# Performance work log

Hardware: AMD Instinct MI355X
Metric: run time of the kernel (lower is better)

Reference implementation:

```python
import jax, jax.numpy as jnp
import numpy as np

EPS = 1e-8  # torch.cosine_similarity default eps


def setup_inputs() -> dict:
    key = jax.random.key(0)
    k1, k2, k3, k4 = jax.random.split(key, 4)
    S, M, N, D = 512, 256, 100000, 1024
    query_hidden = jax.random.normal(k1, (S, D), dtype=jnp.float32)
    bank = jax.random.normal(k2, (N, D), dtype=jnp.float32)
    bank_labels = jax.random.uniform(k3, (N,), dtype=jnp.float32)
    bucket_idx = jax.random.randint(k4, (S, M), 0, N, dtype=jnp.int64)
    return {
        "query_hidden": query_hidden,
        "bank": bank,
        "bank_labels": bank_labels,
        "bucket_idx": bucket_idx,
        "k": 5,
    }


def reference(query_hidden, bank, bank_labels, bucket_idx, k):
    # Gather candidate embeddings / labels per query token: [S, M, D], [S, M]
    cand = bank[bucket_idx]
    cand_labels = bank_labels[bucket_idx]

    # Cosine similarity (torch semantics: / max(||x||, eps) per vector)
    q_norm = jnp.maximum(jnp.linalg.norm(query_hidden, axis=-1, keepdims=True), EPS)
    c_norm = jnp.maximum(jnp.linalg.norm(cand, axis=-1), EPS)  # [S, M]
    dots = jnp.einsum("sd,smd->sm", query_hidden, cand)
    sims = dots / (q_norm * c_norm)

    # Top-k per token, mean of the selected labels, then round
    _, top_idx = jax.lax.top_k(sims, k)  # [S, k]
    sel_labels = jnp.take_along_axis(cand_labels, top_idx, axis=-1)  # [S, k]
    labels = jnp.round(jnp.mean(sel_labels, axis=-1))  # [S]
    return labels
```

## Files before the change

### kernel.cpp

```cpp
#include <hip/hip_runtime.h>

#define SQ_ 512
#define MQ_ 256
#define DQ_ 1024
#define KQ_ 5
#define EPSQ 1e-8f

__global__ void qnorm_kernel(const float* __restrict__ q, float* __restrict__ qn) {
    int wave = (int)((blockIdx.x * blockDim.x + threadIdx.x) >> 6);
    int lane = threadIdx.x & 63;
    if (wave >= SQ_) return;
    const float4* row = (const float4*)(q + (size_t)wave * DQ_);
    float sq = 0.f;
#pragma unroll
    for (int i = 0; i < DQ_ / 4 / 64; ++i) {
        float4 v = row[lane + i * 64];
        sq += v.x * v.x + v.y * v.y + v.z * v.z + v.w * v.w;
    }
#pragma unroll
    for (int off = 32; off; off >>= 1) sq += __shfl_xor(sq, off);
    if (lane == 0) qn[wave] = fmaxf(sqrtf(sq), EPSQ);
}

__global__ void sim_kernel(const float* __restrict__ q,
                           const float* __restrict__ bank,
                           const float* __restrict__ labels,
                           const int* __restrict__ bidx,
                           const float* __restrict__ qn,
                           float* __restrict__ sims,
                           float* __restrict__ slab) {
    long long gw = (long long)(blockIdx.x * (long long)blockDim.x + threadIdx.x) >> 6;
    int lane = threadIdx.x & 63;
    if (gw >= (long long)SQ_ * MQ_) return;
    int s = (int)(gw >> 8);
    int idx = bidx[gw];
    const float4* crow = (const float4*)(bank + (long long)idx * DQ_);
    const float4* qrow = (const float4*)(q + (size_t)s * DQ_);
    float dot = 0.f, sq = 0.f;
#pragma unroll
    for (int i = 0; i < 4; ++i) {
        int j = lane + i * 64;
        float4 c = crow[j];
        float4 qq = qrow[j];
        dot += c.x * qq.x + c.y * qq.y + c.z * qq.z + c.w * qq.w;
        sq  += c.x * c.x + c.y * c.y + c.z * c.z + c.w * c.w;
    }
#pragma unroll
    for (int off = 32; off; off >>= 1) {
        dot += __shfl_xor(dot, off);
        sq  += __shfl_xor(sq, off);
    }
    if (lane == 0) {
        float cn = fmaxf(sqrtf(sq), EPSQ);
        sims[gw] = dot / (qn[s] * cn);
        slab[gw] = labels[idx];
    }
}

__global__ void topk_kernel(const float* __restrict__ sims,
                            const float* __restrict__ slab,
                            float* __restrict__ out) {
    int gw = (int)((blockIdx.x * blockDim.x + threadIdx.x) >> 6);
    int lane = threadIdx.x & 63;
    if (gw >= SQ_) return;
    const float* srow = sims + (size_t)gw * MQ_;
    const float* lrow = slab + (size_t)gw * MQ_;
    float v[4];
#pragma unroll
    for (int i = 0; i < 4; ++i) v[i] = srow[lane + i * 64];
    float sum = 0.f;
    for (int t = 0; t < KQ_; ++t) {
        float bv = v[0];
        int bi = lane;
#pragma unroll
        for (int i = 1; i < 4; ++i) {
            if (v[i] > bv) { bv = v[i]; bi = lane + i * 64; }
        }
#pragma unroll
        for (int off = 32; off; off >>= 1) {
            float ov = __shfl_xor(bv, off);
            int oi = __shfl_xor(bi, off);
            if (ov > bv || (ov == bv && oi < bi)) { bv = ov; bi = oi; }
        }
        sum += lrow[bi];
        if ((bi & 63) == lane && (bi >> 6) >= 0) {
            v[bi >> 6] = -2.0f;
        }
    }
    if (lane == 0) out[gw] = rintf(sum / (float)KQ_);
}

extern "C" void kernel_launch(void* const* d_in, const int* in_sizes, int n_in,
                              void* d_out, int out_size, void* d_ws, size_t ws_size,
                              hipStream_t stream) {
    const float* q      = (const float*)d_in[0];
    const float* bank   = (const float*)d_in[1];
    const float* labels = (const float*)d_in[2];
    const int*   bidx   = (const int*)d_in[3];

    float* out = (float*)d_out;

    float* sims = (float*)d_ws;
    float* slab = sims + (size_t)SQ_ * MQ_;
    float* qn   = slab + (size_t)SQ_ * MQ_;

    qnorm_kernel<<<SQ_ / 4, 256, 0, stream>>>(q, qn);

    sim_kernel<<<(SQ_ * MQ_) / 4, 256, 0, stream>>>(q, bank, labels, bidx, qn, sims, slab);

    topk_kernel<<<SQ_ / 4, 256, 0, stream>>>(sims, slab, out);
}
```

Before: 90.61 us.

## Bucket-sort gather indices by bank region to improve cache locality

Adds a counting-sort pass (histogram, scan, atomic scatter) that reorders the (query, candidate) pairs by bank row index in 128-row buckets before the similarity kernel. Waves processing nearby bank rows then run together, so repeated bank rows (each row is hit about 1.3 times on average) and adjacent rows are more likely to be served from cache instead of HBM. The cost is four extra launches, global atomics, and scattered writes of sims and labels plus scattered query-row reads. Bank index arithmetic bits >> 7 gives up to 782 buckets, within the 1024-bucket histogram.

Result: slower. 176.4 us (+94.7%).

```diff
diff --git a/kernel.cpp b/kernel.cpp
--- a/kernel.cpp
+++ b/kernel.cpp
@@ -2,9 +2,45 @@
 
 #define SQ_ 512
 #define MQ_ 256
+#define SM_ (SQ_ * MQ_)
 #define DQ_ 1024
 #define KQ_ 5
 #define EPSQ 1e-8f
+#define NB_ 1024
+
+__global__ void zero_hist_kernel(int* __restrict__ hist) {
+    int i = blockIdx.x * blockDim.x + threadIdx.x;
+    if (i < NB_) hist[i] = 0;
+}
+
+__global__ void hist_kernel(const int* __restrict__ bidx, int* __restrict__ hist) {
+    int i = blockIdx.x * blockDim.x + threadIdx.x;
+    if (i < SM_) atomicAdd(&hist[bidx[i] >> 7], 1);
+}
+
+__global__ void scan_kernel(const int* __restrict__ hist, int* __restrict__ cursor) {
+    __shared__ int tmp[NB_];
+    int tid = threadIdx.x;
+    tmp[tid] = hist[tid];
+    __syncthreads();
+    for (int off = 1; off < NB_; off <<= 1) {
+        int v = (tid >= off) ? tmp[tid - off] : 0;
+        __syncthreads();
+        tmp[tid] += v;
+        __syncthreads();
+    }
+    cursor[tid] = (tid == 0) ? 0 : tmp[tid - 1];
+}
+
+__global__ void scatter_kernel(const int* __restrict__ bidx, int* __restrict__ cursor,
+                               int* __restrict__ sidx, int* __restrict__ ssm) {
+    int i = blockIdx.x * blockDim.x + threadIdx.x;
+    if (i >= SM_) return;
+    int idx = bidx[i];
+    int pos = atomicAdd(&cursor[idx >> 7], 1);
+    sidx[pos] = idx;
+    ssm[pos] = i;
+}
 
 __global__ void qnorm_kernel(const float* __restrict__ q, float* __restrict__ qn) {
     int wave = (int)((blockIdx.x * blockDim.x + threadIdx.x) >> 6);
@@ -25,15 +61,17 @@
 __global__ void sim_kernel(const float* __restrict__ q,
                            const float* __restrict__ bank,
                            const float* __restrict__ labels,
-                           const int* __restrict__ bidx,
+                           const int* __restrict__ sidx,
+                           const int* __restrict__ ssm,
                            const float* __restrict__ qn,
                            float* __restrict__ sims,
                            float* __restrict__ slab) {
     long long gw = (long long)(blockIdx.x * (long long)blockDim.x + threadIdx.x) >> 6;
     int lane = threadIdx.x & 63;
-    if (gw >= (long long)SQ_ * MQ_) return;
-    int s = (int)(gw >> 8);
-    int idx = bidx[gw];
+    if (gw >= (long long)SM_) return;
+    int idx = sidx[gw];
+    int sm  = ssm[gw];
+    int s = sm >> 8;
     const float4* crow = (const float4*)(bank + (long long)idx * DQ_);
     const float4* qrow = (const float4*)(q + (size_t)s * DQ_);
     float dot = 0.f, sq = 0.f;
@@ -52,8 +90,8 @@
     }
     if (lane == 0) {
         float cn = fmaxf(sqrtf(sq), EPSQ);
-        sims[gw] = dot / (qn[s] * cn);
-        slab[gw] = labels[idx];
+        sims[sm] = dot / (qn[s] * cn);
+        slab[sm] = labels[idx];
     }
 }
 
@@ -83,9 +121,7 @@
             if (ov > bv || (ov == bv && oi < bi)) { bv = ov; bi = oi; }
         }
         sum += lrow[bi];
-        if ((bi & 63) == lane && (bi >> 6) >= 0) {
-            v[bi >> 6] = -2.0f;
-        }
+        if ((bi & 63) == lane) v[bi >> 6] = -2.0f;
     }
     if (lane == 0) out[gw] = rintf(sum / (float)KQ_);
 }
@@ -100,13 +136,22 @@
 
     float* out = (float*)d_out;
 
-    float* sims = (float*)d_ws;
-    float* slab = sims + (size_t)SQ_ * MQ_;
-    float* qn   = slab + (size_t)SQ_ * MQ_;
+    float* sims   = (float*)d_ws;
+    float* slab   = sims + SM_;
+    float* qn     = slab + SM_;
+    int*   hist   = (int*)(qn + SQ_);
+    int*   cursor = hist + NB_;
+    int*   sidx   = cursor + NB_;
+    int*   ssm    = sidx + SM_;
+
+    zero_hist_kernel<<<(NB_ + 255) / 256, 256, 0, stream>>>(hist);
+    hist_kernel<<<(SM_ + 255) / 256, 256, 0, stream>>>(bidx, hist);
+    scan_kernel<<<1, NB_, 0, stream>>>(hist, cursor);
+    scatter_kernel<<<(SM_ + 255) / 256, 256, 0, stream>>>(bidx, cursor, sidx, ssm);
 
     qnorm_kernel<<<SQ_ / 4, 256, 0, stream>>>(q, qn);
 
-    sim_kernel<<<(SQ_ * MQ_) / 4, 256, 0, stream>>>(q, bank, labels, bidx, qn, sims, slab);
+    sim_kernel<<<SM_ / 4, 256, 0, stream>>>(q, bank, labels, sidx, ssm, qn, sims, slab);
 
     topk_kernel<<<SQ_ / 4, 256, 0, stream>>>(sims, slab, out);
 }
```

## Fuse qnorm, similarity and top-k into one per-token kernel

Applied to the files above, without the earlier changes.

Replaces three kernels with a single kernel that launches one 1024-thread block per query token. The query row is held in registers and its norm is computed once per block. Each wave computes similarities for 16 gathered candidates into shared memory, and wave 0 then runs the top-k and label average. This removes the global sims and label buffers and two launches, at the cost of fewer, longer-running blocks that may expose less memory parallelism for the random bank gathers.

Measured after the change: 85.15 us. 6.0% less time.

```diff
diff --git a/kernel.cpp b/kernel.cpp
--- a/kernel.cpp
+++ b/kernel.cpp
@@ -6,88 +6,89 @@
 #define KQ_ 5
 #define EPSQ 1e-8f
 
-__global__ void qnorm_kernel(const float* __restrict__ q, float* __restrict__ qn) {
-    int wave = (int)((blockIdx.x * blockDim.x + threadIdx.x) >> 6);
-    int lane = threadIdx.x & 63;
-    if (wave >= SQ_) return;
-    const float4* row = (const float4*)(q + (size_t)wave * DQ_);
-    float sq = 0.f;
+__global__ __launch_bounds__(1024) void fused_kernel(
+    const float* __restrict__ q,
+    const float* __restrict__ bank,
+    const float* __restrict__ labels,
+    const int* __restrict__ bidx,
+    float* __restrict__ out) {
+    __shared__ float s_sims[MQ_];
+    __shared__ int   s_idx[MQ_];
+
+    int s    = blockIdx.x;
+    int tid  = threadIdx.x;
+    int wave = tid >> 6;
+    int lane = tid & 63;
+
+    if (tid < MQ_) s_idx[tid] = bidx[(size_t)s * MQ_ + tid];
+    __syncthreads();
+
+    const float4* qrow = (const float4*)(q + (size_t)s * DQ_);
+    float4 q0 = qrow[lane];
+    float4 q1 = qrow[lane + 64];
+    float4 q2 = qrow[lane + 128];
+    float4 q3 = qrow[lane + 192];
+
+    float qsq = q0.x * q0.x + q0.y * q0.y + q0.z * q0.z + q0.w * q0.w
+              + q1.x * q1.x + q1.y * q1.y + q1.z * q1.z + q1.w * q1.w
+              + q2.x * q2.x + q2.y * q2.y + q2.z * q2.z + q2.w * q2.w
+              + q3.x * q3.x + q3.y * q3.y + q3.z * q3.z + q3.w * q3.w;
 #pragma unroll
-    for (int i = 0; i < DQ_ / 4 / 64; ++i) {
-        float4 v = row[lane + i * 64];
-        sq += v.x * v.x + v.y * v.y + v.z * v.z + v.w * v.w;
-    }
-#pragma unroll
-    for (int off = 32; off; off >>= 1) sq += __shfl_xor(sq, off);
-    if (lane == 0) qn[wave] = fmaxf(sqrtf(sq), EPSQ);
-}
+    for (int off = 32; off; off >>= 1) qsq += __shfl_xor(qsq, off);
+    float qn = fmaxf(sqrtf(qsq), EPSQ);
 
-__global__ void sim_kernel(const float* __restrict__ q,
-                           const float* __restrict__ bank,
-                           const float* __restrict__ labels,
-                           const int* __restrict__ bidx,
-                           const float* __restrict__ qn,
-                           float* __restrict__ sims,
-                           float* __restrict__ slab) {
-    long long gw = (long long)(blockIdx.x * (long long)blockDim.x + threadIdx.x) >> 6;
-    int lane = threadIdx.x & 63;
-    if (gw >= (long long)SQ_ * MQ_) return;
-    int s = (int)(gw >> 8);
-    int idx = bidx[gw];
-    const float4* crow = (const float4*)(bank + (long long)idx * DQ_);
-    const float4* qrow = (const float4*)(q + (size_t)s * DQ_);
-    float dot = 0.f, sq = 0.f;
-#pragma unroll
-    for (int i = 0; i < 4; ++i) {
-        int j = lane + i * 64;
-        float4 c = crow[j];
-        float4 qq = qrow[j];
-        dot += c.x * qq.x + c.y * qq.y + c.z * qq.z + c.w * qq.w;
-        sq  += c.x * c.x + c.y * c.y + c.z * c.z + c.w * c.w;
-    }
-#pragma unroll
-    for (int off = 32; off; off >>= 1) {
-        dot += __shfl_xor(dot, off);
-        sq  += __shfl_xor(sq, off);
-    }
-    if (lane == 0) {
-        float cn = fmaxf(sqrtf(sq), EPSQ);
-        sims[gw] = dot / (qn[s] * cn);
-        slab[gw] = labels[idx];
-    }
-}
-
-__global__ void topk_kernel(const float* __restrict__ sims,
-                            const float* __restrict__ slab,
-                            float* __restrict__ out) {
-    int gw = (int)((blockIdx.x * blockDim.x + threadIdx.x) >> 6);
-    int lane = threadIdx.x & 63;
-    if (gw >= SQ_) return;
-    const float* srow = sims + (size_t)gw * MQ_;
-    const float* lrow = slab + (size_t)gw * MQ_;
-    float v[4];
-#pragma unroll
-    for (int i = 0; i < 4; ++i) v[i] = srow[lane + i * 64];
-    float sum = 0.f;
-    for (int t = 0; t < KQ_; ++t) {
-        float bv = v[0];
-        int bi = lane;
-#pragma unroll
-        for (int i = 1; i < 4; ++i) {
-            if (v[i] > bv) { bv = v[i]; bi = lane + i * 64; }
-        }
+    for (int t = 0; t < MQ_ / 16; ++t) {
+        int m = wave * 16 + t;
+        int idx = s_idx[m];
+        const float4* crow = (const float4*)(bank + (size_t)idx * DQ_);
+        float4 c0 = crow[lane];
+        float4 c1 = crow[lane + 64];
+        float4 c2 = crow[lane + 128];
+        float4 c3 = crow[lane + 192];
+        float dot = 0.f, sq = 0.f;
+        dot += c0.x * q0.x + c0.y * q0.y + c0.z * q0.z + c0.w * q0.w;
+        sq  += c0.x * c0.x + c0.y * c0.y + c0.z * c0.z + c0.w * c0.w;
+        dot += c1.x * q1.x + c1.y * q1.y + c1.z * q1.z + c1.w * q1.w;
+        sq  += c1.x * c1.x + c1.y * c1.y + c1.z * c1.z + c1.w * c1.w;
+        dot += c2.x * q2.x + c2.y * q2.y + c2.z * q2.z + c2.w * q2.w;
+        sq  += c2.x * c2.x + c2.y * c2.y + c2.z * c2.z + c2.w * c2.w;
+        dot += c3.x * q3.x + c3.y * q3.y + c3.z * q3.z + c3.w * q3.w;
+        sq  += c3.x * c3.x + c3.y * c3.y + c3.z * c3.z + c3.w * c3.w;
 #pragma unroll
         for (int off = 32; off; off >>= 1) {
-            float ov = __shfl_xor(bv, off);
-            int oi = __shfl_xor(bi, off);
-            if (ov > bv || (ov == bv && oi < bi)) { bv = ov; bi = oi; }
+            dot += __shfl_xor(dot, off);
+            sq  += __shfl_xor(sq, off);
         }
-        sum += lrow[bi];
-        if ((bi & 63) == lane && (bi >> 6) >= 0) {
-            v[bi >> 6] = -2.0f;
+        if (lane == 0) {
+            float cn = fmaxf(sqrtf(sq), EPSQ);
+            s_sims[m] = dot / (qn * cn);
         }
     }
-    if (lane == 0) out[gw] = rintf(sum / (float)KQ_);
+    __syncthreads();
+
+    if (wave == 0) {
+        float v[4];
+#pragma unroll
+        for (int i = 0; i < 4; ++i) v[i] = s_sims[lane + i * 64];
+        float sum = 0.f;
+        for (int t = 0; t < KQ_; ++t) {
+            float bv = v[0];
+            int bi = lane;
+#pragma unroll
+            for (int i = 1; i < 4; ++i) {
+                if (v[i] > bv) { bv = v[i]; bi = lane + i * 64; }
+            }
+#pragma unroll
+            for (int off = 32; off; off >>= 1) {
+                float ov = __shfl_xor(bv, off);
+                int oi = __shfl_xor(bi, off);
+                if (ov > bv || (ov == bv && oi < bi)) { bv = ov; bi = oi; }
+            }
+            sum += labels[s_idx[bi]];
+            if ((bi & 63) == lane) v[bi >> 6] = -2.0f;
+        }
+        if (lane == 0) out[s] = rintf(sum / (float)KQ_);
+    }
 }
 
 extern "C" void kernel_launch(void* const* d_in, const int* in_sizes, int n_in,
@@ -97,16 +98,7 @@
     const float* bank   = (const float*)d_in[1];
     const float* labels = (const float*)d_in[2];
     const int*   bidx   = (const int*)d_in[3];
-
     float* out = (float*)d_out;
 
-    float* sims = (float*)d_ws;
-    float* slab = sims + (size_t)SQ_ * MQ_;
-    float* qn   = slab + (size_t)SQ_ * MQ_;
-
-    qnorm_kernel<<<SQ_ / 4, 256, 0, stream>>>(q, qn);
-
-    sim_kernel<<<(SQ_ * MQ_) / 4, 256, 0, stream>>>(q, bank, labels, bidx, qn, sims, slab);
-
-    topk_kernel<<<SQ_ / 4, 256, 0, stream>>>(sims, slab, out);
+    fused_kernel<<<SQ_, 1024, 0, stream>>>(q, bank, labels, bidx, out);
 }
```
